# Performance work log

Measured on AMD Instinct MI355X. Metric: run time of the kernel, lower is better.

The kernel has to match this reference:

```python
import jax, jax.numpy as jnp
import numpy as np
import math

IMG_W, IMG_H = 800, 320
N_POINTS = 72
N_STRIPS = 71
S = 36   # sample_points
P = 192  # n_priors
C = 64   # prior_fea_channels == fc_hidden_dim
B = 32

SAMPLE_X_IDX = (np.linspace(0, 1, S) * N_STRIPS).astype(np.int64)
PRIOR_FEAT_YS = np.flip(1.0 - SAMPLE_X_IDX.astype(np.float32) / N_STRIPS).copy()
PRIOR_YS = np.linspace(1, 0, N_POINTS, dtype=np.float32)


def _init_priors():
    emb = np.zeros((P, 3), np.float32)
    left = P // 8
    bottom = P * 3 // 4
    strip = 0.5 / (left // 2 - 1)
    bstrip = 1.0 / (bottom // 4 + 1)
    for i in range(left):
        emb[i] = ((i // 2) * strip, 0.0, 0.16 if i % 2 == 0 else 0.32)
    for i in range(left, left + bottom):
        emb[i] = (0.0, ((i - left) // 4 + 1) * bstrip, 0.2 * (i % 4 + 1))
    for i in range(left + bottom, P):
        emb[i] = (((i - left - bottom) // 2) * strip, 1.0, 0.68 if i % 2 == 0 else 0.84)
    pri = np.zeros((P, 6 + N_POINTS), np.float32)
    pri[:, 2:5] = emb
    pri[:, 6:] = (emb[:, 1:2] * (IMG_W - 1)
                  + (1 - PRIOR_YS[None] - emb[:, 0:1]) * IMG_H / np.tan(emb[:, 2:3] * math.pi + 1e-5)) / (IMG_W - 1)
    return pri.astype(np.float32), pri[:, 6 + SAMPLE_X_IDX].astype(np.float32)


def _bn(x, p):
    # p: (4, C) = gamma, beta, running_mean, running_var; channel axis = 1 (eval mode)
    g, b, m, v = p[0], p[1], p[2], p[3]
    shape = [1] * x.ndim
    shape[1] = -1
    return (x - m.reshape(shape)) * (g.reshape(shape) / jnp.sqrt(v.reshape(shape) + 1e-5)) + b.reshape(shape)


def _conv1d(x, w, pad):
    # x (N, Cin, L), w (Cout, Cin, K); the torch module uses (9,1) conv on (...,36,1)
    return jax.lax.conv_general_dilated(x, w, (1,), [(pad, pad)],
                                        dimension_numbers=('NCH', 'OIH', 'NCH'))


def _grid_sample(img, gx, gy):
    # F.grid_sample: bilinear, align_corners=True, padding_mode='zeros'
    # img (B,C,H,W); gx, gy (B,P,S) in [-1,1] -> out (B,C,P,S)
    b, c, h, w = img.shape
    x = (gx + 1.0) * 0.5 * (w - 1)
    y = (gy + 1.0) * 0.5 * (h - 1)
    x0 = jnp.floor(x)
    y0 = jnp.floor(y)
    imgf = img.reshape(b, c, h * w)

    def gather(xi, yi):
        valid = (xi >= 0) & (xi <= w - 1) & (yi >= 0) & (yi <= h - 1)
        xi_c = jnp.clip(xi, 0, w - 1).astype(jnp.int32)
        yi_c = jnp.clip(yi, 0, h - 1).astype(jnp.int32)
        idx = yi_c * w + xi_c
        v = jax.vmap(lambda f, ix: f[:, ix])(imgf, idx)  # (B,C,P,S)
        return v * valid[:, None].astype(img.dtype)

    wx = x - x0
    wy = y - y0
    return (gather(x0, y0) * ((1 - wx) * (1 - wy))[:, None]
            + gather(x0 + 1, y0) * (wx * (1 - wy))[:, None]
            + gather(x0, y0 + 1) * ((1 - wx) * wy)[:, None]
            + gather(x0 + 1, y0 + 1) * (wx * wy)[:, None])


def _resize_nearest(x, oh, ow):
    # torch F.interpolate default: nearest, idx = floor(i * in / out)
    b, c, h, w = x.shape
    ri = (jnp.arange(oh) * h) // oh
    rj = (jnp.arange(ow) * w) // ow
    return x[:, :, ri][:, :, :, rj]


def _forward(x0, x1, x2, priors0, priors_feat0, conv_w, bn_conv, cat_w0, cat_w1, cat_w2,
             bn_cat, fkey_w, bn_key, fval_w, fval_b, fq_w, fq_b, attnW_w, attnW_b,
             fc_w, fc_b, ln_g, ln_b, mlp_w, mlp_b, reg_w, reg_b, cls_w, cls_b):
    feats = [x2, x1, x0]  # batch_features = x[-3:] reversed -> coarsest first
    b = x0.shape[0]
    prior_ys = jnp.asarray(PRIOR_YS)
    feat_ys = jnp.asarray(PRIOR_FEAT_YS)
    sx_idx = jnp.asarray(SAMPLE_X_IDX)
    priors = jnp.broadcast_to(priors0, (b, P, 6 + N_POINTS))
    priors_feat = jnp.broadcast_to(priors_feat0, (b, P, S))
    cat_ws = [cat_w0, cat_w1, cat_w2]
    stage_rois = []
    preds = []
    for stage in range(3):
        fmap = feats[stage]
        prior_xs = priors_feat[:, :, ::-1]  # torch.flip(dim=2)
        gx = prior_xs * 2.0 - 1.0
        gy = jnp.broadcast_to((feat_ys * 2.0 - 1.0)[None, None, :], (b, P, S))
        pooled = _grid_sample(fmap, gx, gy)                 # (B,C,P,S)
        pooled = pooled.transpose(0, 2, 1, 3).reshape(b * P, C, S)
        stage_rois.append(pooled)
        # ROIGather.roi_fea: per-stage (9,1) conv + BN + ReLU, then cat conv
        trans = [jax.nn.relu(_bn(_conv1d(stage_rois[i], conv_w[i], 4), bn_conv[i]))
                 for i in range(stage + 1)]
        cat = jnp.concatenate(trans, axis=1)
        cat = jax.nn.relu(_bn(_conv1d(cat, cat_ws[stage], 4), bn_cat[stage]))  # (B*P,C,S)
        # fc + LayerNorm + ReLU
        roi = cat.reshape(b * P, C * S) @ fc_w + fc_b
        mu = roi.mean(-1, keepdims=True)
        var = roi.var(-1, keepdims=True)
        roi = (roi - mu) / jnp.sqrt(var + 1e-5) * ln_g + ln_b
        roi = jax.nn.relu(roi).reshape(b, P, C)
        # attention: grouped-conv1d query (per-prior scalar), key/value on resized map
        query = jax.nn.relu(roi * fq_w[None, :, None] + fq_b[None, :, None])
        key = jax.nn.relu(_bn(jnp.einsum('bchw,oc->bohw', fmap, fkey_w), bn_key))
        key = _resize_nearest(key, 10, 25).reshape(b, C, 250)
        value = jnp.einsum('bchw,oc->bohw', fmap, fval_w) + fval_b[None, :, None, None]
        value = _resize_nearest(value, 10, 25).reshape(b, C, 250)
        sim = jax.nn.softmax(jnp.einsum('bpc,bck->bpk', query, key) * (C ** -0.5), axis=-1)
        context = jnp.einsum('bpk,bck->bpc', sim, value)
        context = context * attnW_w[None, :, None] + attnW_b[None, :, None]
        roi = roi + context  # dropout inactive in eval
        # heads (source bug: reg and cls share the SAME Linear applied twice)
        f = roi.reshape(b * P, C)
        h = jax.nn.relu(f @ mlp_w + mlp_b)
        h = jax.nn.relu(h @ mlp_w + mlp_b)
        cls_logits = (h @ cls_w + cls_b).reshape(b, P, 2)
        reg = (h @ reg_w + reg_b).reshape(b, P, 4 + N_POINTS)
        p2 = priors[..., 2] + reg[..., 0]
        p3 = priors[..., 3] + reg[..., 1]
        p4 = priors[..., 4] + reg[..., 2]
        p5 = reg[..., 3]
        geom = (p3[..., None] * (IMG_W - 1)
                + (1.0 - prior_ys[None, None, :] - p2[..., None]) * IMG_H
                / jnp.tan(p4[..., None] * math.pi + 1e-5)) / (IMG_W - 1)
        head = jnp.stack([cls_logits[..., 0], cls_logits[..., 1], p2, p3, p4, p5], axis=-1)
        pred = jnp.concatenate([head, geom + reg[..., 4:]], axis=-1)
        preds.append(pred)
        if stage != 2:
            lines = jax.lax.stop_gradient(jnp.concatenate([head, geom], axis=-1))
            priors = lines
            priors_feat = lines[..., 6 + sx_idx]
    return jnp.stack(preds, axis=0)  # (3, B, P, 78)


def setup_inputs() -> dict:
    key = jax.random.key(0)
    ks = list(jax.random.split(key, 24))
    f32 = jnp.float32
    rn = lambda k, sh, s: jax.random.normal(k, sh, dtype=f32) * s

    def bn_p(k, *lead):
        k1, k2, k3, k4 = jax.random.split(k, 4)
        g = 0.75 + 0.5 * jax.random.uniform(k1, lead + (C,), dtype=f32)
        b = 0.1 * jax.random.normal(k2, lead + (C,), dtype=f32)
        m = 0.1 * jax.random.normal(k3, lead + (C,), dtype=f32)
        v = 0.75 + 0.5 * jax.random.uniform(k4, lead + (C,), dtype=f32)
        return jnp.stack([g, b, m, v], axis=-2)  # (..., 4, C)

    pri, prif = _init_priors()
    return {
        'x0': rn(ks[0], (B, C, IMG_H // 8, IMG_W // 8), 1.0),
        'x1': rn(ks[1], (B, C, IMG_H // 16, IMG_W // 16), 1.0),
        'x2': rn(ks[2], (B, C, IMG_H // 32, IMG_W // 32), 1.0),
        'priors0': jnp.asarray(pri),
        'priors_feat0': jnp.asarray(prif),
        'conv_w': rn(ks[3], (3, C, C, 9), 0.04),
        'bn_conv': bn_p(ks[4], 3),
        'cat_w0': rn(ks[5], (C, C, 9), 0.04),
        'cat_w1': rn(ks[6], (C, 2 * C, 9), 0.03),
        'cat_w2': rn(ks[7], (C, 3 * C, 9), 0.025),
        'bn_cat': bn_p(ks[8], 3),
        'fkey_w': rn(ks[9], (C, C), 0.12),
        'bn_key': bn_p(ks[10]),
        'fval_w': rn(ks[11], (C, C), 0.12),
        'fval_b': rn(ks[12], (C,), 0.05),
        'fq_w': 1.0 + rn(ks[13], (P,), 0.1),
        'fq_b': rn(ks[14], (P,), 0.05),
        'attnW_w': rn(ks[15], (P,), 0.02),
        'attnW_b': rn(ks[16], (P,), 0.02),
        'fc_w': rn(ks[17], (C * S, C), 0.02),
        'fc_b': rn(ks[18], (C,), 0.02),
        'ln_g': jnp.ones((C,), f32),
        'ln_b': jnp.zeros((C,), f32),
        'mlp_w': rn(ks[19], (C, C), 0.12),
        'mlp_b': rn(ks[20], (C,), 0.02),
        'reg_w': rn(ks[21], (C, 4 + N_POINTS), 0.001),
        'reg_b': rn(ks[22], (4 + N_POINTS,), 0.001),
        'cls_w': rn(ks[23], (C, 2), 0.001),
        'cls_b': jnp.zeros((2,), f32),
    }


def reference(x0, x1, x2, priors0, priors_feat0, conv_w, bn_conv, cat_w0, cat_w1, cat_w2,
              bn_cat, fkey_w, bn_key, fval_w, fval_b, fq_w, fq_b, attnW_w, attnW_b,
              fc_w, fc_b, ln_g, ln_b, mlp_w, mlp_b, reg_w, reg_b, cls_w, cls_b):
    return _forward(x0, x1, x2, priors0, priors_feat0, conv_w, bn_conv, cat_w0, cat_w1,
                    cat_w2, bn_cat, fkey_w, bn_key, fval_w, fval_b, fq_w, fq_b,
                    attnW_w, attnW_b, fc_w, fc_b, ln_g, ln_b, mlp_w, mlp_b,
                    reg_w, reg_b, cls_w, cls_b)
```

## Files before the change

kernel.cpp:

```cpp
#include <hip/hip_runtime.h>
#include <hip/hip_bf16.h>
#include <math.h>

typedef __hip_bfloat16 bf16;
typedef __attribute__((ext_vector_type(8))) short short8v;
typedef __attribute__((ext_vector_type(4))) float float4v;

static constexpr int kB = 32;
static constexpr int kP = 192;
static constexpr int kS = 36;
static constexpr int kC = 64;
static constexpr int kRows = kB * kP;
static constexpr float kPI = 3.14159265358979323846f;

__device__ __constant__ int d_SX[36] = {
  0,2,4,6,8,10,12,14,16,18,20,22,24,26,28,30,32,34,
  36,38,40,42,44,46,48,50,52,54,56,58,60,62,64,66,68,71};

__device__ __forceinline__ float b2f(bf16 v) { return __bfloat162float(v); }
__device__ __forceinline__ unsigned short f2bu(float f) {
  bf16 h = __float2bfloat16(f);
  return *reinterpret_cast<unsigned short*>(&h);
}
__device__ __forceinline__ float su2f(unsigned short u) {
  bf16 t; *reinterpret_cast<unsigned short*>(&t) = u; return __bfloat162float(t);
}
#define MFMA16 __builtin_amdgcn_mfma_f32_16x16x32_bf16

__device__ __forceinline__ void wprep_one(
    int d, const float* __restrict__ src, bf16* __restrict__ dst, int CI)
{
  int j   = d & 7;
  int l   = (d >> 3) & 63;
  int wid = (d >> 9) & 3;
  int r   = d >> 11;
  int nchi = CI >> 5;
  int chi = r % nchi, t = r / nchi;
  int co = wid * 16 + (l & 15);
  int ci = chi * 32 + 8 * (l >> 4) + j;
  dst[d] = __float2bfloat16(src[(co * CI + ci) * 9 + t]);
}

__global__ __launch_bounds__(256) void k_prep_all(
    const float* __restrict__ conv_w,
    const float* __restrict__ cat_w0, const float* __restrict__ cat_w1,
    const float* __restrict__ cat_w2,
    const float* __restrict__ fc_w, const float* __restrict__ mlp_w,
    const float* __restrict__ regw, const float* __restrict__ regb,
    const float* __restrict__ clsw, const float* __restrict__ clsb,
    const float* __restrict__ fkeyw, const float* __restrict__ fvalw,
    bf16* __restrict__ wtr0, bf16* __restrict__ wtr1, bf16* __restrict__ wtr2,
    bf16* __restrict__ wcat0, bf16* __restrict__ wcat1, bf16* __restrict__ wcat2,
    bf16* __restrict__ wfc, bf16* __restrict__ mlpwT,
    bf16* __restrict__ rcT, float* __restrict__ rcb,
    float* __restrict__ fkeyT, float* __restrict__ fvalT)
{
  int d = blockIdx.x * 256 + threadIdx.x;
  if (d < 36864)        { wprep_one(d, conv_w,               wtr0, 64); return; }
  d -= 36864;
  if (d < 36864)        { wprep_one(d, conv_w + 36864,       wtr1, 64); return; }
  d -= 36864;
  if (d < 36864)        { wprep_one(d, conv_w + 2*36864,     wtr2, 64); return; }
  d -= 36864;
  if (d < 36864)        { wprep_one(d, cat_w0, wcat0, 64);  return; }
  d -= 36864;
  if (d < 73728)        { wprep_one(d, cat_w1, wcat1, 128); return; }
  d -= 73728;
  if (d < 110592)       { wprep_one(d, cat_w2, wcat2, 192); return; }
  d -= 110592;
  if (d < 147456) {
    int j    = d & 7;
    int l    = (d >> 3) & 63;
    int tile = (d >> 9) & 3;
    int kk   = d >> 11;
    int cout = tile * 16 + (l & 15);
    int k    = kk * 32 + 8 * (l >> 4) + j;
    int c = k & 63, s = k >> 6;
    wfc[d] = __float2bfloat16(fc_w[(c * kS + s) * kC + cout]);
    return;
  }
  d -= 147456;
  if (d < 4096) {
    int co = d >> 6, ci = d & 63;
    mlpwT[d] = __float2bfloat16(mlp_w[ci * 64 + co]);
    return;
  }
  d -= 4096;
  if (d < 5120) {
    int o = d >> 6, ci = d & 63;
    float v = (o < 76) ? regw[ci * 76 + o] : (o < 78 ? clsw[ci * 2 + (o - 76)] : 0.f);
    rcT[d] = __float2bfloat16(v);
    if (d < 80) rcb[d] = (d < 76) ? regb[d] : (d < 78 ? clsb[d - 76] : 0.f);
    return;
  }
  d -= 5120;
  if (d < 4096) {
    int c = d >> 6, co = d & 63;
    fkeyT[d] = fkeyw[co * 64 + c];
    return;
  }
  d -= 4096;
  if (d < 4096) {
    int c = d >> 6, co = d & 63;
    fvalT[d] = fvalw[co * 64 + c];
  }
}

__global__ __launch_bounds__(256) void k_transpose3(
    const float* __restrict__ x2, const float* __restrict__ x1, const float* __restrict__ x0,
    bf16* __restrict__ f0, bf16* __restrict__ f1, bf16* __restrict__ f2)
{
  __shared__ float tile[64][65];
  int byA = blockIdx.x;
  const float* src; bf16* dst; int h, w;
  if (byA < kB*10)            { src = x2; dst = f0; h = 10; w = 25;  }
  else if (byA < kB*30)       { src = x1; dst = f1; h = 20; w = 50;  byA -= kB*10; }
  else                        { src = x0; dst = f2; h = 40; w = 100; byA -= kB*30; }
  const int b = byA / h, y = byA % h;
  const int lane = threadIdx.x & 63, wq = threadIdx.x >> 6;
  for (int x0i = 0; x0i < w; x0i += 64) {
    #pragma unroll
    for (int cc = 0; cc < 16; ++cc) {
      int c = wq * 16 + cc;
      int x = x0i + lane;
      if (x < w) tile[c][lane] = src[((size_t)(b*kC + c)*h + y)*w + x];
    }
    __syncthreads();
    #pragma unroll
    for (int xx = 0; xx < 16; ++xx) {
      int x = x0i + wq * 16 + xx;
      if (x < w) dst[((size_t)(b*h + y)*w + x)*kC + lane] = __float2bfloat16(tile[lane][wq*16 + xx]);
    }
    __syncthreads();
  }
}

__global__ __launch_bounds__(256) void k_keyval3(
    const bf16* __restrict__ f0, const bf16* __restrict__ f1, const bf16* __restrict__ f2,
    const float* __restrict__ fkeyT, const float* __restrict__ bnk,
    const float* __restrict__ fvalT, const float* __restrict__ fvalb,
    bf16* __restrict__ k0, bf16* __restrict__ v0,
    bf16* __restrict__ k1, bf16* __restrict__ v1,
    bf16* __restrict__ k2, bf16* __restrict__ v2)
{
  const int tid = threadIdx.x, lane = tid & 63, grp = tid >> 6;
  int blk = blockIdx.x;
  const int stage = blk / (kB*64);
  blk -= stage * (kB*64);
  const bf16* fmapT; bf16 *key_pc, *val_ck; int h, w;
  if (stage == 0)      { fmapT = f0; key_pc = k0; val_ck = v0; h = 10; w = 25;  }
  else if (stage == 1) { fmapT = f1; key_pc = k1; val_ck = v1; h = 20; w = 50;  }
  else                 { fmapT = f2; key_pc = k2; val_ck = v2; h = 40; w = 100; }
  const int b = blk >> 6, pg = blk & 63;
  const int pos = pg * 4 + grp;
  __shared__ float fv[4][64];
  const bool valid = (pos < 250);
  if (valid) {
    int i = pos / 25, j = pos % 25;
    int yi = (i * h) / 10, xj = (j * w) / 25;
    fv[grp][lane] = b2f(fmapT[((size_t)(b*h + yi)*w + xj)*kC + lane]);
  }
  __syncthreads();
  if (valid) {
    float ka = 0.f, va = 0.f;
    #pragma unroll 8
    for (int c = 0; c < kC; ++c) {
      float f = fv[grp][c];
      ka += f * fkeyT[c*64 + lane];
      va += f * fvalT[c*64 + lane];
    }
    float g = bnk[lane], bb = bnk[kC + lane];
    float m = bnk[2*kC + lane], v = bnk[3*kC + lane];
    float sc = g / sqrtf(v + 1e-5f), sh = bb - m * sc;
    key_pc[((size_t)b*256 + pos)*kC + lane] = __float2bfloat16(fmaxf(ka*sc + sh, 0.f));
    val_ck[((size_t)b*kC + lane)*256 + pos] = __float2bfloat16(va + fvalb[lane]);
  } else {
    key_pc[((size_t)b*256 + pos)*kC + lane] = __float2bfloat16(0.f);
    val_ck[((size_t)b*kC + lane)*256 + pos] = __float2bfloat16(0.f);
  }
}

__global__ __launch_bounds__(256) void k_trans(
    const bf16* __restrict__ fmapT, int h, int w,
    const float* __restrict__ pfeat0, const float* __restrict__ pfeatw, int stage,
    const bf16* __restrict__ wfrag,
    const float* __restrict__ bnp,
    bf16* __restrict__ transOut)
{
  __shared__ __align__(16) bf16 poolT[2][56][64];
  __shared__ float bsc[kC], bsh[kC];
  const int tid = threadIdx.x;
  const int row0 = blockIdx.x * 2, b = row0 / kP;

  if (tid < kC) {
    float g = bnp[tid], bb = bnp[kC + tid];
    float m = bnp[2*kC + tid], v = bnp[3*kC + tid];
    float sc = g / sqrtf(v + 1e-5f);
    bsc[tid] = sc; bsh[tid] = bb - m * sc;
  }
  unsigned int* pz = (unsigned int*)&poolT[0][0][0];
  for (int e = tid; e < 2*56*32; e += 256) pz[e] = 0u;
  __syncthreads();

  const int lc = tid & 7;
  for (int idx = tid >> 3; idx < 2*kS; idx += 32) {
    int r2 = idx / kS, s = idx % kS;
    int row = row0 + r2, p = row % kP;
    float px = (stage == 0) ? pfeat0[p*kS + (kS-1-s)] : pfeatw[row*kS + (kS-1-s)];
    float fy = 1.0f - (float)d_SX[kS-1-s] / 71.0f;
    float x = px * (float)(w - 1);
    float y = fy * (float)(h - 1);
    float x0f = floorf(x), y0f = floorf(y);
    float wx = x - x0f, wy = y - y0f;
    int xi = (int)x0f, yi = (int)y0f;
    float a8[8];
    #pragma unroll
    for (int j = 0; j < 8; ++j) a8[j] = 0.f;
    #pragma unroll
    for (int cy = 0; cy < 2; ++cy) {
      #pragma unroll
      for (int cx = 0; cx < 2; ++cx) {
        int xx = xi + cx, yy = yi + cy;
        if (xx >= 0 && xx < w && yy >= 0 && yy < h) {
          float wgt = (cx ? wx : 1.f - wx) * (cy ? wy : 1.f - wy);
          short8v v = *(const short8v*)&fmapT[((size_t)(b*h + yy)*w + xx)*kC + lc*8];
          #pragma unroll
          for (int j = 0; j < 8; ++j)
            a8[j] += su2f((unsigned short)v[j]) * wgt;
        }
      }
    }
    uint4 pk;
    pk.x = (unsigned)f2bu(a8[0]) | ((unsigned)f2bu(a8[1]) << 16);
    pk.y = (unsigned)f2bu(a8[2]) | ((unsigned)f2bu(a8[3]) << 16);
    pk.z = (unsigned)f2bu(a8[4]) | ((unsigned)f2bu(a8[5]) << 16);
    pk.w = (unsigned)f2bu(a8[6]) | ((unsigned)f2bu(a8[7]) << 16);
    int lr = s + 4;
    *reinterpret_cast<uint4*>(&poolT[r2][lr][((lc + lr) & 7)*8]) = pk;
  }
  __syncthreads();

  const int wv = tid >> 6, lane = tid & 63;
  const int r2 = wv & 1, cp = wv >> 1;
  const int lm = lane & 15, lq = lane >> 4;
  float4v acc[2][3] = {{{0,0,0,0},{0,0,0,0},{0,0,0,0}},{{0,0,0,0},{0,0,0,0},{0,0,0,0}}};
  #pragma unroll
  for (int t = 0; t < 9; ++t) {
    #pragma unroll
    for (int chi = 0; chi < 2; ++chi) {
      short8v a0 = *(const short8v*)&wfrag[(((t*2 + chi)*4 + cp*2 + 0)*64 + lane)*8];
      short8v a1 = *(const short8v*)&wfrag[(((t*2 + chi)*4 + cp*2 + 1)*64 + lane)*8];
      #pragma unroll
      for (int nt = 0; nt < 3; ++nt) {
        int rr = nt*16 + lm + t;
        int sl = chi*4 + lq;
        short8v bb = *(const short8v*)&poolT[r2][rr][((sl + rr) & 7)*8];
        acc[0][nt] = MFMA16(a0, bb, acc[0][nt], 0, 0, 0);
        acc[1][nt] = MFMA16(a1, bb, acc[1][nt], 0, 0, 0);
      }
    }
  }
  #pragma unroll
  for (int c2 = 0; c2 < 2; ++c2) {
    const int c4 = (cp*2 + c2)*16 + 4*lq;
    float s0 = bsc[c4], s1 = bsc[c4+1], s2 = bsc[c4+2], s3 = bsc[c4+3];
    float h0 = bsh[c4], h1 = bsh[c4+1], h2 = bsh[c4+2], h3 = bsh[c4+3];
    #pragma unroll
    for (int nt = 0; nt < 3; ++nt) {
      int s = nt*16 + lm;
      if (s < kS) {
        uint2 pk;
        pk.x = (unsigned)f2bu(fmaxf(acc[c2][nt][0]*s0 + h0, 0.f))
             | ((unsigned)f2bu(fmaxf(acc[c2][nt][1]*s1 + h1, 0.f)) << 16);
        pk.y = (unsigned)f2bu(fmaxf(acc[c2][nt][2]*s2 + h2, 0.f))
             | ((unsigned)f2bu(fmaxf(acc[c2][nt][3]*s3 + h3, 0.f)) << 16);
        *reinterpret_cast<uint2*>(&transOut[((size_t)(row0+r2)*kS + s)*kC + c4]) = pk;
      }
    }
  }
}

template<int NCI>
__global__ __launch_bounds__(256) void k_catconv(
    const bf16* __restrict__ t0, const bf16* __restrict__ t1, const bf16* __restrict__ t2,
    const bf16* __restrict__ wfrag,
    const float* __restrict__ bnp, bf16* __restrict__ catOut)
{
  constexpr int CB = NCI/8;
  __shared__ __align__(16) bf16 poolT[2][56][NCI];
  __shared__ float bsc[kC], bsh[kC];
  const int tid = threadIdx.x;
  const int row0 = blockIdx.x * 2;
  if (tid < kC) {
    float g = bnp[tid], bb = bnp[kC + tid];
    float m = bnp[2*kC + tid], v = bnp[3*kC + tid];
    float sc = g / sqrtf(v + 1e-5f);
    bsc[tid] = sc; bsh[tid] = bb - m * sc;
  }
  unsigned int* pz = (unsigned int*)&poolT[0][0][0];
  for (int e = tid; e < 2*56*NCI/2; e += 256) pz[e] = 0u;
  __syncthreads();

  const bf16* tb[3] = {t0, t1, t2};
  for (int cc = tid; cc < 2*kS*CB; cc += 256) {
    int r2 = cc / (kS*CB), rem = cc % (kS*CB);
    int s = rem / CB, cb = rem % CB;
    int ch = cb * 8, i = ch >> 6, c = ch & 63;
    const short8v* src = (const short8v*)&tb[i][((size_t)(row0+r2)*kS + s)*kC + c];
    int lr = s + 4;
    int sl = (cb & ~7) | ((cb + lr) & 7);
    *(short8v*)&poolT[r2][lr][sl*8] = *src;
  }
  __syncthreads();

  const int wv = tid >> 6, lane = tid & 63;
  const int r2 = wv & 1, cp = wv >> 1;
  const int lm = lane & 15, lq = lane >> 4;
  float4v acc[2][3] = {{{0,0,0,0},{0,0,0,0},{0,0,0,0}},{{0,0,0,0},{0,0,0,0},{0,0,0,0}}};
  #pragma unroll
  for (int t = 0; t < 9; ++t) {
    #pragma unroll
    for (int chi = 0; chi < NCI/32; ++chi) {
      short8v a0 = *(const short8v*)&wfrag[(((t*(NCI/32) + chi)*4 + cp*2 + 0)*64 + lane)*8];
      short8v a1 = *(const short8v*)&wfrag[(((t*(NCI/32) + chi)*4 + cp*2 + 1)*64 + lane)*8];
      #pragma unroll
      for (int nt = 0; nt < 3; ++nt) {
        int rr = nt*16 + lm + t;
        int sl0 = chi*4 + lq;
        int sl = (sl0 & ~7) | ((sl0 + rr) & 7);
        short8v bb = *(const short8v*)&poolT[r2][rr][sl*8];
        acc[0][nt] = MFMA16(a0, bb, acc[0][nt], 0, 0, 0);
        acc[1][nt] = MFMA16(a1, bb, acc[1][nt], 0, 0, 0);
      }
    }
  }
  #pragma unroll
  for (int c2 = 0; c2 < 2; ++c2) {
    const int c4 = (cp*2 + c2)*16 + 4*lq;
    float s0 = bsc[c4], s1 = bsc[c4+1], s2 = bsc[c4+2], s3 = bsc[c4+3];
    float h0 = bsh[c4], h1 = bsh[c4+1], h2 = bsh[c4+2], h3 = bsh[c4+3];
    #pragma unroll
    for (int nt = 0; nt < 3; ++nt) {
      int s = nt*16 + lm;
      if (s < kS) {
        uint2 pk;
        pk.x = (unsigned)f2bu(fmaxf(acc[c2][nt][0]*s0 + h0, 0.f))
             | ((unsigned)f2bu(fmaxf(acc[c2][nt][1]*s1 + h1, 0.f)) << 16);
        pk.y = (unsigned)f2bu(fmaxf(acc[c2][nt][2]*s2 + h2, 0.f))
             | ((unsigned)f2bu(fmaxf(acc[c2][nt][3]*s3 + h3, 0.f)) << 16);
        *reinterpret_cast<uint2*>(&catOut[((size_t)(row0+r2)*kS + s)*kC + c4]) = pk;
      }
    }
  }
}

__global__ __launch_bounds__(256) void k_tail(
    const bf16* __restrict__ catOut, const bf16* __restrict__ wfc,
    const float* __restrict__ fcb, const float* __restrict__ lng, const float* __restrict__ lnb,
    const bf16* __restrict__ key_pc, const bf16* __restrict__ val_ck,
    const float* __restrict__ fqw, const float* __restrict__ fqb,
    const float* __restrict__ aww, const float* __restrict__ awb,
    const bf16* __restrict__ mlpwT, const float* __restrict__ mlpb,
    const bf16* __restrict__ rcT, const float* __restrict__ rcb,
    const float* __restrict__ priors0, const float* __restrict__ priw_in, int stage,
    float* __restrict__ out, float* __restrict__ priw_out, float* __restrict__ pfeat_out)
{
  __shared__ __align__(16) float partS[4][16][68];
  __shared__ __align__(16) float roiL[12][68];
  __shared__ __align__(16) bf16 q[16][72];
  __shared__ __align__(16) bf16 P[16][264];
  __shared__ float rsum[16];
  __shared__ __align__(16) bf16 r2b[16][72];
  __shared__ __align__(16) bf16 h1l[16][72];
  __shared__ __align__(16) bf16 h2l[16][72];
  __shared__ float regc[12][84];
  __shared__ float ev[12][8];

  const int tid = threadIdx.x;
  const int blk = blockIdx.x, b = blk >> 4, tile = blk & 15;
  const int p0 = tile * 12;
  const int lane = tid & 63, wq = tid >> 6;
  const int lm = lane & 15, lq = lane >> 4;
  float (*S)[264] = (float (*)[264])&partS[0][0][0];

  { unsigned* z1 = (unsigned*)&q[0][0];
    for (int e = tid; e < 16*72/2; e += 256) z1[e] = 0u;
    unsigned* z2 = (unsigned*)&r2b[0][0];
    for (int e = tid; e < 16*72/2; e += 256) z2[e] = 0u; }

  {
    float4v fa[4] = {{0,0,0,0},{0,0,0,0},{0,0,0,0},{0,0,0,0}};
    int r0c = p0 + lm; if (r0c > p0 + 11) r0c = p0 + 11;
    const bf16* bb0 = catOut + (size_t)(b*kP + r0c) * 2304 + lq * 8;
    for (int kk = wq * 18; kk < wq * 18 + 18; ++kk) {
      short8v bf0 = *(const short8v*)&bb0[kk * 32];
      #pragma unroll
      for (int t = 0; t < 4; ++t) {
        short8v afrag = *(const short8v*)&wfc[((kk*4 + t)*64 + lane)*8];
        fa[t] = MFMA16(afrag, bf0, fa[t], 0, 0, 0);
      }
    }
    #pragma unroll
    for (int t = 0; t < 4; ++t)
      *(float4v*)&partS[wq][lm][t*16 + lq*4] = fa[t];
  }
  __syncthreads();
  for (int r = wq; r < 12; r += 4) {
    float v = partS[0][r][lane] + partS[1][r][lane] + partS[2][r][lane] + partS[3][r][lane]
            + fcb[lane];
    float s1 = v, s2 = v * v;
    #pragma unroll
    for (int m = 32; m; m >>= 1) { s1 += __shfl_xor(s1, m, 64); s2 += __shfl_xor(s2, m, 64); }
    float mu = s1 * (1.f/64.f);
    float var = s2 * (1.f/64.f) - mu * mu;
    float y = fmaxf((v - mu) * rsqrtf(var + 1e-5f) * lng[lane] + lnb[lane], 0.f);
    roiL[r][lane] = y;
    int p = p0 + r;
    q[r][lane] = __float2bfloat16(fmaxf(y * fqw[p] + fqb[p], 0.f));
  }
  __syncthreads();

  {
    float4v acc[4] = {{0,0,0,0},{0,0,0,0},{0,0,0,0},{0,0,0,0}};
    #pragma unroll
    for (int ks = 0; ks < 2; ++ks) {
      short8v aq0 = *(const short8v*)&q[lm][ks*32 + 8*lq];
      #pragma unroll
      for (int nt = 0; nt < 4; ++nt) {
        int pos = (wq*4 + nt)*16 + lm;
        short8v bk = *(const short8v*)&key_pc[((size_t)(b*256 + pos))*kC + ks*32 + 8*lq];
        acc[nt] = MFMA16(aq0, bk, acc[nt], 0, 0, 0);
      }
    }
    #pragma unroll
    for (int nt = 0; nt < 4; ++nt)
      #pragma unroll
      for (int r = 0; r < 4; ++r)
        S[lq*4 + r][(wq*4 + nt)*16 + lm] = acc[nt][r] * 0.125f;
  }
  __syncthreads();

  {
    int r = tid >> 4, g = tid & 15;
    float mx = -1e30f;
    #pragma unroll 16
    for (int k = 0; k < 16; ++k) { int c = g + 16*k; if (c < 250) mx = fmaxf(mx, S[r][c]); }
    #pragma unroll
    for (int m = 1; m < 16; m <<= 1) mx = fmaxf(mx, __shfl_xor(mx, m, 64));
    float sum = 0.f;
    #pragma unroll 16
    for (int k = 0; k < 16; ++k) {
      int c = g + 16*k;
      float e = 0.f;
      if (c < 250) { e = expf(S[r][c] - mx); sum += e; }
      P[r][c] = __float2bfloat16(e);
    }
    #pragma unroll
    for (int m = 1; m < 16; m <<= 1) sum += __shfl_xor(sum, m, 64);
    if (g == 0) rsum[r] = sum;
  }
  __syncthreads();

  {
    float4v acc = {0,0,0,0};
    #pragma unroll
    for (int ks = 0; ks < 8; ++ks) {
      short8v bv = *(const short8v*)&val_ck[((size_t)(b*kC + wq*16 + lm))*256 + ks*32 + 8*lq];
      short8v ap0 = *(const short8v*)&P[lm][ks*32 + 8*lq];
      acc = MFMA16(ap0, bv, acc, 0, 0, 0);
    }
    #pragma unroll
    for (int r = 0; r < 4; ++r) {
      int pl = lq*4 + r;
      if (pl < 12) {
        int p = p0 + pl, c = wq*16 + lm;
        float ctx = acc[r] / rsum[pl];
        r2b[pl][c] = __float2bfloat16(roiL[pl][c] + ctx * aww[p] + awb[p]);
      }
    }
  }
  __syncthreads();

  {
    float4v acc = {0,0,0,0};
    #pragma unroll
    for (int ks = 0; ks < 2; ++ks) {
      short8v a0 = *(const short8v*)&r2b[lm][ks*32 + 8*lq];
      short8v bw = *(const short8v*)&mlpwT[(wq*16 + lm)*kC + ks*32 + 8*lq];
      acc = MFMA16(a0, bw, acc, 0, 0, 0);
    }
    #pragma unroll
    for (int r = 0; r < 4; ++r) {
      int rw = lq*4 + r, col = wq*16 + lm;
      h1l[rw][col] = __float2bfloat16(fmaxf(acc[r] + mlpb[col], 0.f));
    }
  }
  __syncthreads();
  {
    float4v acc = {0,0,0,0};
    #pragma unroll
    for (int ks = 0; ks < 2; ++ks) {
      short8v a0 = *(const short8v*)&h1l[lm][ks*32 + 8*lq];
      short8v bw = *(const short8v*)&mlpwT[(wq*16 + lm)*kC + ks*32 + 8*lq];
      acc = MFMA16(a0, bw, acc, 0, 0, 0);
    }
    #pragma unroll
    for (int r = 0; r < 4; ++r) {
      int rw = lq*4 + r, col = wq*16 + lm;
      h2l[rw][col] = __float2bfloat16(fmaxf(acc[r] + mlpb[col], 0.f));
    }
  }
  __syncthreads();
  for (int ntile = wq; ntile < 5; ntile += 4) {
    float4v acc = {0,0,0,0};
    #pragma unroll
    for (int ks = 0; ks < 2; ++ks) {
      short8v a0 = *(const short8v*)&h2l[lm][ks*32 + 8*lq];
      short8v bw = *(const short8v*)&rcT[(ntile*16 + lm)*kC + ks*32 + 8*lq];
      acc = MFMA16(a0, bw, acc, 0, 0, 0);
    }
    #pragma unroll
    for (int r = 0; r < 4; ++r) {
      int rw = lq*4 + r, col = ntile*16 + lm;
      if (rw < 12) regc[rw][col] = acc[r] + rcb[col];
    }
  }
  __syncthreads();

  if (tid < 12) {
    int r = tid, p = p0 + r, grow = b*kP + p;
    float pr2, pr3, pr4;
    if (stage == 0) {
      pr2 = priors0[p*78 + 2]; pr3 = priors0[p*78 + 3]; pr4 = priors0[p*78 + 4];
    } else {
      const float* pw = priw_in + (size_t)grow * 78;
      pr2 = pw[2]; pr3 = pw[3]; pr4 = pw[4];
    }
    float p2 = pr2 + regc[r][0], p3 = pr3 + regc[r][1];
    float p4 = pr4 + regc[r][2], p5 = regc[r][3];
    ev[r][0] = p2; ev[r][1] = p3; ev[r][2] = p4; ev[r][3] = p5;
    ev[r][4] = 320.f / tanf(p4 * kPI + 1e-5f);
    ev[r][5] = regc[r][76]; ev[r][6] = regc[r][77];
  }
  __syncthreads();
  for (int e = tid; e < 12*78; e += 256) {
    int r = e / 78, o = e % 78;
    int p = p0 + r, grow = b*kP + p;
    float p2 = ev[r][0], p3 = ev[r][1], t320 = ev[r][4];
    float g = 0.f, v;
    if (o >= 6) g = (p3 * 799.f + ((float)(o-6) / 71.f - p2) * t320) / 799.f;
    if      (o == 0) v = ev[r][5];
    else if (o == 1) v = ev[r][6];
    else if (o == 2) v = p2;
    else if (o == 3) v = p3;
    else if (o == 4) v = ev[r][2];
    else if (o == 5) v = ev[r][3];
    else             v = g + regc[r][4 + (o - 6)];
    out[((size_t)(stage*kB + b)*kP + p) * 78 + o] = v;
    if (stage < 2) priw_out[(size_t)grow*78 + o] = (o < 6) ? v : g;
  }
  if (stage < 2) {
    for (int e = tid; e < 12*kS; e += 256) {
      int r = e / kS, si = e % kS;
      int grow = b*kP + p0 + r;
      float p2 = ev[r][0], p3 = ev[r][1], t320 = ev[r][4];
      pfeat_out[(size_t)grow*kS + si] =
          (p3 * 799.f + ((float)d_SX[si] / 71.f - p2) * t320) / 799.f;
    }
  }
}

extern "C" void kernel_launch(void* const* d_in, const int* in_sizes, int n_in,
                              void* d_out, int out_size, void* d_ws, size_t ws_size,
                              hipStream_t stream) {
  const float* x0      = (const float*)d_in[0];
  const float* x1      = (const float*)d_in[1];
  const float* x2      = (const float*)d_in[2];
  const float* priors0 = (const float*)d_in[3];
  const float* pfeat0  = (const float*)d_in[4];
  const float* conv_w  = (const float*)d_in[5];
  const float* bn_conv = (const float*)d_in[6];
  const float* cat_w[3]= {(const float*)d_in[7], (const float*)d_in[8], (const float*)d_in[9]};
  const float* bn_cat  = (const float*)d_in[10];
  const float* fkey_w  = (const float*)d_in[11];
  const float* bn_key  = (const float*)d_in[12];
  const float* fval_w  = (const float*)d_in[13];
  const float* fval_b  = (const float*)d_in[14];
  const float* fq_w    = (const float*)d_in[15];
  const float* fq_b    = (const float*)d_in[16];
  const float* attnW_w = (const float*)d_in[17];
  const float* attnW_b = (const float*)d_in[18];
  const float* fc_w    = (const float*)d_in[19];
  const float* fc_b    = (const float*)d_in[20];
  const float* ln_g    = (const float*)d_in[21];
  const float* ln_b    = (const float*)d_in[22];
  const float* mlp_w   = (const float*)d_in[23];
  const float* mlp_b   = (const float*)d_in[24];
  const float* reg_w   = (const float*)d_in[25];
  const float* reg_b   = (const float*)d_in[26];
  const float* cls_w   = (const float*)d_in[27];
  const float* cls_b   = (const float*)d_in[28];
  float* out = (float*)d_out;

  char* ws = (char*)d_ws;
  size_t off = 0;
  auto alloc = [&](size_t bytes) { void* pp = ws + off; off += (bytes + 255) & ~(size_t)255; return pp; };
  bf16* trans[3];
  for (int i = 0; i < 3; ++i) trans[i] = (bf16*)alloc((size_t)kRows * 2304 * sizeof(bf16));
  bf16*  catout = (bf16*) alloc((size_t)kRows * 2304 * sizeof(bf16));
  bf16*  key_pc[3]; bf16* val_ck[3];
  for (int i = 0; i < 3; ++i) {
    key_pc[i] = (bf16*)alloc((size_t)kB * 256 * kC * sizeof(bf16));
    val_ck[i] = (bf16*)alloc((size_t)kB * kC * 256 * sizeof(bf16));
  }
  float* priwA  = (float*)alloc((size_t)kRows * 78 * sizeof(float));
  float* priwB  = (float*)alloc((size_t)kRows * 78 * sizeof(float));
  float* pfw    = (float*)alloc((size_t)kRows * kS * sizeof(float));
  bf16* wtr[3], *wcat[3];
  const int catCI[3] = {64, 128, 192};
  for (int i = 0; i < 3; ++i) wtr[i]  = (bf16*)alloc((size_t)64*64*9 * sizeof(bf16));
  for (int i = 0; i < 3; ++i) wcat[i] = (bf16*)alloc((size_t)64*catCI[i]*9 * sizeof(bf16));
  bf16* wfc    = (bf16*)alloc((size_t)2304*64 * sizeof(bf16));
  bf16* mlpwT  = (bf16*)alloc((size_t)64*64 * sizeof(bf16));
  bf16* rcT    = (bf16*)alloc((size_t)80*64 * sizeof(bf16));
  float* rcb   = (float*)alloc((size_t)80 * sizeof(float));
  float* fkeyT = (float*)alloc((size_t)64*64 * sizeof(float));
  float* fvalT = (float*)alloc((size_t)64*64 * sizeof(float));
  const int hd[3] = {10, 20, 40}, wd[3] = {25, 50, 100};
  bf16* fmapT[3];
  for (int i = 0; i < 3; ++i)
    fmapT[i] = (bf16*)alloc((size_t)kB * hd[i] * wd[i] * kC * sizeof(bf16));
  (void)ws_size; (void)in_sizes; (void)n_in; (void)out_size;

  k_prep_all<<<(496640 + 255)/256, 256, 0, stream>>>(
      conv_w, cat_w[0], cat_w[1], cat_w[2], fc_w, mlp_w, reg_w, reg_b, cls_w, cls_b,
      fkey_w, fval_w,
      wtr[0], wtr[1], wtr[2], wcat[0], wcat[1], wcat[2], wfc, mlpwT, rcT, rcb,
      fkeyT, fvalT);
  k_transpose3<<<kB*70, 256, 0, stream>>>(x2, x1, x0, fmapT[0], fmapT[1], fmapT[2]);
  k_keyval3<<<3*kB*64, 256, 0, stream>>>(fmapT[0], fmapT[1], fmapT[2],
                                         fkeyT, bn_key, fvalT, fval_b,
                                         key_pc[0], val_ck[0], key_pc[1], val_ck[1],
                                         key_pc[2], val_ck[2]);

  for (int st = 0; st < 3; ++st) {
    const int h = hd[st], w = wd[st];
    const float* priw_in  = (st == 1) ? priwA : priwB;
    float*       priw_out = (st == 0) ? priwA : priwB;
    k_trans<<<kRows/2, 256, 0, stream>>>(fmapT[st], h, w, pfeat0, pfw, st,
                                         wtr[st], bn_conv + st*4*kC, trans[st]);
    if (st == 0)
      k_catconv<64><<<kRows/2, 256, 0, stream>>>(trans[0], trans[1], trans[2], wcat[0],
                                                 bn_cat + st*4*kC, catout);
    else if (st == 1)
      k_catconv<128><<<kRows/2, 256, 0, stream>>>(trans[0], trans[1], trans[2], wcat[1],
                                                  bn_cat + st*4*kC, catout);
    else
      k_catconv<192><<<kRows/2, 256, 0, stream>>>(trans[0], trans[1], trans[2], wcat[2],
                                                  bn_cat + st*4*kC, catout);
    k_tail<<<kB*16, 256, 0, stream>>>(catout, wfc, fc_b, ln_g, ln_b,
                                      key_pc[st], val_ck[st], fq_w, fq_b, attnW_w, attnW_b,
                                      mlpwT, mlp_b, rcT, rcb,
                                      priors0, priw_in, st, out, priw_out, pfw);
  }
}
```

Baseline: 390.3 us.

## Fuse per-stage sampling conv with concatenation conv in one kernel

Merges the per-stage grid-sample plus 9-tap conv kernel with the following concatenation conv kernel. The freshly computed stage feature stays in shared memory as the last channel block of the concat input. Earlier stages' features are loaded from global memory, and the final stage no longer writes its intermediate feature to global memory. This removes one launch per stage and a global round trip of the transformed features. In exchange the kernel uses more shared memory and registers, which may reduce occupancy.

```diff
diff --git a/kernel.cpp b/kernel.cpp
--- a/kernel.cpp
+++ b/kernel.cpp
@@ -94,16 +94,9 @@
     return;
   }
   d -= 5120;
-  if (d < 4096) {
-    int c = d >> 6, co = d & 63;
-    fkeyT[d] = fkeyw[co * 64 + c];
-    return;
-  }
+  if (d < 4096) { int c = d >> 6, co = d & 63; fkeyT[d] = fkeyw[co * 64 + c]; return; }
   d -= 4096;
-  if (d < 4096) {
-    int c = d >> 6, co = d & 63;
-    fvalT[d] = fvalw[co * 64 + c];
-  }
+  if (d < 4096) { int c = d >> 6, co = d & 63; fvalT[d] = fvalw[co * 64 + c]; }
 }
 
 __global__ __launch_bounds__(256) void k_transpose3(
@@ -180,175 +173,178 @@
   }
 }
 
-__global__ __launch_bounds__(256) void k_trans(
+template<int ST>
+__global__ __launch_bounds__(256) void k_transcat(
     const bf16* __restrict__ fmapT, int h, int w,
-    const float* __restrict__ pfeat0, const float* __restrict__ pfeatw, int stage,
-    const bf16* __restrict__ wfrag,
-    const float* __restrict__ bnp,
-    bf16* __restrict__ transOut)
+    const float* __restrict__ pfeat0, const float* __restrict__ pfeatw,
+    const bf16* __restrict__ wtr,
+    const float* __restrict__ bnpT,
+    const bf16* __restrict__ t0, const bf16* __restrict__ t1,
+    const bf16* __restrict__ wcat,
+    const float* __restrict__ bnpC,
+    bf16* __restrict__ transOut,
+    bf16* __restrict__ catOut)
 {
-  __shared__ __align__(16) bf16 poolT[2][56][64];
-  __shared__ float bsc[kC], bsh[kC];
+  constexpr int NCI = 64 * (ST + 1);
+  __shared__ __align__(16) bf16 pool[2][56][NCI];
+  __shared__ float bscT[64], bshT[64], bscC[64], bshC[64];
   const int tid = threadIdx.x;
   const int row0 = blockIdx.x * 2, b = row0 / kP;
 
-  if (tid < kC) {
-    float g = bnp[tid], bb = bnp[kC + tid];
-    float m = bnp[2*kC + tid], v = bnp[3*kC + tid];
+  if (tid < 64) {
+    float g = bnpT[tid], bb = bnpT[64+tid], m = bnpT[128+tid], v = bnpT[192+tid];
     float sc = g / sqrtf(v + 1e-5f);
-    bsc[tid] = sc; bsh[tid] = bb - m * sc;
-  }
-  unsigned int* pz = (unsigned int*)&poolT[0][0][0];
-  for (int e = tid; e < 2*56*32; e += 256) pz[e] = 0u;
-  __syncthreads();
-
-  const int lc = tid & 7;
-  for (int idx = tid >> 3; idx < 2*kS; idx += 32) {
-    int r2 = idx / kS, s = idx % kS;
-    int row = row0 + r2, p = row % kP;
-    float px = (stage == 0) ? pfeat0[p*kS + (kS-1-s)] : pfeatw[row*kS + (kS-1-s)];
-    float fy = 1.0f - (float)d_SX[kS-1-s] / 71.0f;
-    float x = px * (float)(w - 1);
-    float y = fy * (float)(h - 1);
-    float x0f = floorf(x), y0f = floorf(y);
-    float wx = x - x0f, wy = y - y0f;
-    int xi = (int)x0f, yi = (int)y0f;
-    float a8[8];
-    #pragma unroll
-    for (int j = 0; j < 8; ++j) a8[j] = 0.f;
-    #pragma unroll
-    for (int cy = 0; cy < 2; ++cy) {
+    bscT[tid] = sc; bshT[tid] = bb - m * sc;
+    g = bnpC[tid]; bb = bnpC[64+tid]; m = bnpC[128+tid]; v = bnpC[192+tid];
+    sc = g / sqrtf(v + 1e-5f);
+    bscC[tid] = sc; bshC[tid] = bb - m * sc;
+  }
+  {
+    unsigned* pz = (unsigned*)&pool[0][0][0];
+    constexpr int ND = NCI/2;
+    for (int e = tid; e < 2*20*ND; e += 256) {
+      int r2 = e / (20*ND), rem = e % (20*ND);
+      int pr = rem / ND, cd = rem % ND;
+      int lr = (pr < 4) ? pr : pr + 36;
+      pz[((size_t)r2*56 + lr)*ND + cd] = 0u;
+    }
+  }
+
+  {
+    const int lc = tid & 7;
+    for (int idx = tid >> 3; idx < 2*kS; idx += 32) {
+      int r2 = idx / kS, s = idx % kS;
+      int row = row0 + r2, p = row % kP;
+      float px = (ST == 0) ? pfeat0[p*kS + (kS-1-s)] : pfeatw[row*kS + (kS-1-s)];
+      float fy = 1.0f - (float)d_SX[kS-1-s] / 71.0f;
+      float x = px * (float)(w - 1);
+      float y = fy * (float)(h - 1);
+      float x0f = floorf(x), y0f = floorf(y);
+      float wx = x - x0f, wy = y - y0f;
+      int xi = (int)x0f, yi = (int)y0f;
+      float a8[8];
       #pragma unroll
-      for (int cx = 0; cx < 2; ++cx) {
-        int xx = xi + cx, yy = yi + cy;
-        if (xx >= 0 && xx < w && yy >= 0 && yy < h) {
-          float wgt = (cx ? wx : 1.f - wx) * (cy ? wy : 1.f - wy);
-          short8v v = *(const short8v*)&fmapT[((size_t)(b*h + yy)*w + xx)*kC + lc*8];
-          #pragma unroll
-          for (int j = 0; j < 8; ++j)
-            a8[j] += su2f((unsigned short)v[j]) * wgt;
+      for (int j = 0; j < 8; ++j) a8[j] = 0.f;
+      #pragma unroll
+      for (int cy = 0; cy < 2; ++cy) {
+        #pragma unroll
+        for (int cx = 0; cx < 2; ++cx) {
+          int xx = xi + cx, yy = yi + cy;
+          if (xx >= 0 && xx < w && yy >= 0 && yy < h) {
+            float wgt = (cx ? wx : 1.f - wx) * (cy ? wy : 1.f - wy);
+            short8v v = *(const short8v*)&fmapT[((size_t)(b*h + yy)*w + xx)*kC + lc*8];
+            #pragma unroll
+            for (int j = 0; j < 8; ++j)
+              a8[j] += su2f((unsigned short)v[j]) * wgt;
+          }
         }
       }
-    }
-    uint4 pk;
-    pk.x = (unsigned)f2bu(a8[0]) | ((unsigned)f2bu(a8[1]) << 16);
-    pk.y = (unsigned)f2bu(a8[2]) | ((unsigned)f2bu(a8[3]) << 16);
-    pk.z = (unsigned)f2bu(a8[4]) | ((unsigned)f2bu(a8[5]) << 16);
-    pk.w = (unsigned)f2bu(a8[6]) | ((unsigned)f2bu(a8[7]) << 16);
-    int lr = s + 4;
-    *reinterpret_cast<uint4*>(&poolT[r2][lr][((lc + lr) & 7)*8]) = pk;
+      uint4 pk;
+      pk.x = (unsigned)f2bu(a8[0]) | ((unsigned)f2bu(a8[1]) << 16);
+      pk.y = (unsigned)f2bu(a8[2]) | ((unsigned)f2bu(a8[3]) << 16);
+      pk.z = (unsigned)f2bu(a8[4]) | ((unsigned)f2bu(a8[5]) << 16);
+      pk.w = (unsigned)f2bu(a8[6]) | ((unsigned)f2bu(a8[7]) << 16);
+      int lr = s + 4;
+      int slot = 8*ST + ((lc + lr) & 7);
+      *reinterpret_cast<uint4*>(&pool[r2][lr][slot*8]) = pk;
+    }
+  }
+  if (ST > 0) {
+    const bf16* tb[2] = {t0, t1};
+    constexpr int CBp = 8 * ST;
+    for (int cc = tid; cc < 2*kS*CBp; cc += 256) {
+      int r2 = cc / (kS*CBp), rem = cc % (kS*CBp);
+      int s = rem / CBp, cb = rem % CBp;
+      int ch = cb * 8, i = ch >> 6, c = ch & 63;
+      const short8v* src = (const short8v*)&tb[i][((size_t)(row0+r2)*kS + s)*kC + c];
+      int lr = s + 4;
+      int sl = (cb & ~7) | ((cb + lr) & 7);
+      *(short8v*)&pool[r2][lr][sl*8] = *src;
+    }
   }
   __syncthreads();
 
   const int wv = tid >> 6, lane = tid & 63;
-  const int r2 = wv & 1, cp = wv >> 1;
+  const int r2w = wv & 1, cp = wv >> 1;
   const int lm = lane & 15, lq = lane >> 4;
-  float4v acc[2][3] = {{{0,0,0,0},{0,0,0,0},{0,0,0,0}},{{0,0,0,0},{0,0,0,0},{0,0,0,0}}};
+
+  float4v accT[2][3] = {{{0,0,0,0},{0,0,0,0},{0,0,0,0}},{{0,0,0,0},{0,0,0,0},{0,0,0,0}}};
   #pragma unroll
   for (int t = 0; t < 9; ++t) {
     #pragma unroll
     for (int chi = 0; chi < 2; ++chi) {
-      short8v a0 = *(const short8v*)&wfrag[(((t*2 + chi)*4 + cp*2 + 0)*64 + lane)*8];
-      short8v a1 = *(const short8v*)&wfrag[(((t*2 + chi)*4 + cp*2 + 1)*64 + lane)*8];
+      short8v a0 = *(const short8v*)&wtr[(((t*2 + chi)*4 + cp*2 + 0)*64 + lane)*8];
+      short8v a1 = *(const short8v*)&wtr[(((t*2 + chi)*4 + cp*2 + 1)*64 + lane)*8];
       #pragma unroll
       for (int nt = 0; nt < 3; ++nt) {
         int rr = nt*16 + lm + t;
-        int sl = chi*4 + lq;
-        short8v bb = *(const short8v*)&poolT[r2][rr][((sl + rr) & 7)*8];
-        acc[0][nt] = MFMA16(a0, bb, acc[0][nt], 0, 0, 0);
-        acc[1][nt] = MFMA16(a1, bb, acc[1][nt], 0, 0, 0);
-      }
-    }
-  }
+        int slot = 8*ST + (((chi*4 + lq) + rr) & 7);
+        short8v bb = *(const short8v*)&pool[r2w][rr][slot*8];
+        accT[0][nt] = MFMA16(a0, bb, accT[0][nt], 0, 0, 0);
+        accT[1][nt] = MFMA16(a1, bb, accT[1][nt], 0, 0, 0);
+      }
+    }
+  }
+  __syncthreads();
+
   #pragma unroll
   for (int c2 = 0; c2 < 2; ++c2) {
     const int c4 = (cp*2 + c2)*16 + 4*lq;
-    float s0 = bsc[c4], s1 = bsc[c4+1], s2 = bsc[c4+2], s3 = bsc[c4+3];
-    float h0 = bsh[c4], h1 = bsh[c4+1], h2 = bsh[c4+2], h3 = bsh[c4+3];
+    float s0 = bscT[c4], s1 = bscT[c4+1], s2 = bscT[c4+2], s3 = bscT[c4+3];
+    float h0 = bshT[c4], h1 = bshT[c4+1], h2 = bshT[c4+2], h3 = bshT[c4+3];
     #pragma unroll
     for (int nt = 0; nt < 3; ++nt) {
       int s = nt*16 + lm;
       if (s < kS) {
         uint2 pk;
-        pk.x = (unsigned)f2bu(fmaxf(acc[c2][nt][0]*s0 + h0, 0.f))
-             | ((unsigned)f2bu(fmaxf(acc[c2][nt][1]*s1 + h1, 0.f)) << 16);
-        pk.y = (unsigned)f2bu(fmaxf(acc[c2][nt][2]*s2 + h2, 0.f))
-             | ((unsigned)f2bu(fmaxf(acc[c2][nt][3]*s3 + h3, 0.f)) << 16);
-        *reinterpret_cast<uint2*>(&transOut[((size_t)(row0+r2)*kS + s)*kC + c4]) = pk;
-      }
-    }
-  }
-}
-
-template<int NCI>
-__global__ __launch_bounds__(256) void k_catconv(
-    const bf16* __restrict__ t0, const bf16* __restrict__ t1, const bf16* __restrict__ t2,
-    const bf16* __restrict__ wfrag,
-    const float* __restrict__ bnp, bf16* __restrict__ catOut)
-{
-  constexpr int CB = NCI/8;
-  __shared__ __align__(16) bf16 poolT[2][56][NCI];
-  __shared__ float bsc[kC], bsh[kC];
-  const int tid = threadIdx.x;
-  const int row0 = blockIdx.x * 2;
-  if (tid < kC) {
-    float g = bnp[tid], bb = bnp[kC + tid];
-    float m = bnp[2*kC + tid], v = bnp[3*kC + tid];
-    float sc = g / sqrtf(v + 1e-5f);
-    bsc[tid] = sc; bsh[tid] = bb - m * sc;
-  }
-  unsigned int* pz = (unsigned int*)&poolT[0][0][0];
-  for (int e = tid; e < 2*56*NCI/2; e += 256) pz[e] = 0u;
-  __syncthreads();
-
-  const bf16* tb[3] = {t0, t1, t2};
-  for (int cc = tid; cc < 2*kS*CB; cc += 256) {
-    int r2 = cc / (kS*CB), rem = cc % (kS*CB);
-    int s = rem / CB, cb = rem % CB;
-    int ch = cb * 8, i = ch >> 6, c = ch & 63;
-    const short8v* src = (const short8v*)&tb[i][((size_t)(row0+r2)*kS + s)*kC + c];
-    int lr = s + 4;
-    int sl = (cb & ~7) | ((cb + lr) & 7);
-    *(short8v*)&poolT[r2][lr][sl*8] = *src;
-  }
-  __syncthreads();
-
-  const int wv = tid >> 6, lane = tid & 63;
-  const int r2 = wv & 1, cp = wv >> 1;
-  const int lm = lane & 15, lq = lane >> 4;
-  float4v acc[2][3] = {{{0,0,0,0},{0,0,0,0},{0,0,0,0}},{{0,0,0,0},{0,0,0,0},{0,0,0,0}}};
+        pk.x = (unsigned)f2bu(fmaxf(accT[c2][nt][0]*s0 + h0, 0.f))
+             | ((unsigned)f2bu(fmaxf(accT[c2][nt][1]*s1 + h1, 0.f)) << 16);
+        pk.y = (unsigned)f2bu(fmaxf(accT[c2][nt][2]*s2 + h2, 0.f))
+             | ((unsigned)f2bu(fmaxf(accT[c2][nt][3]*s3 + h3, 0.f)) << 16);
+        if (ST < 2)
+          *reinterpret_cast<uint2*>(&transOut[((size_t)(row0+r2w)*kS + s)*kC + c4]) = pk;
+        int ch = 64*ST + c4;
+        int cb2 = ch >> 3, lr = s + 4;
+        int sl = (cb2 & ~7) | ((cb2 + lr) & 7);
+        *reinterpret_cast<uint2*>(&pool[r2w][lr][sl*8 + (ch & 7)]) = pk;
+      }
+    }
+  }
+  __syncthreads();
+
+  float4v accC[2][3] = {{{0,0,0,0},{0,0,0,0},{0,0,0,0}},{{0,0,0,0},{0,0,0,0},{0,0,0,0}}};
   #pragma unroll
   for (int t = 0; t < 9; ++t) {
     #pragma unroll
     for (int chi = 0; chi < NCI/32; ++chi) {
-      short8v a0 = *(const short8v*)&wfrag[(((t*(NCI/32) + chi)*4 + cp*2 + 0)*64 + lane)*8];
-      short8v a1 = *(const short8v*)&wfrag[(((t*(NCI/32) + chi)*4 + cp*2 + 1)*64 + lane)*8];
+      short8v a0 = *(const short8v*)&wcat[(((t*(NCI/32) + chi)*4 + cp*2 + 0)*64 + lane)*8];
+      short8v a1 = *(const short8v*)&wcat[(((t*(NCI/32) + chi)*4 + cp*2 + 1)*64 + lane)*8];
       #pragma unroll
       for (int nt = 0; nt < 3; ++nt) {
         int rr = nt*16 + lm + t;
         int sl0 = chi*4 + lq;
         int sl = (sl0 & ~7) | ((sl0 + rr) & 7);
-        short8v bb = *(const short8v*)&poolT[r2][rr][sl*8];
-        acc[0][nt] = MFMA16(a0, bb, acc[0][nt], 0, 0, 0);
-        acc[1][nt] = MFMA16(a1, bb, acc[1][nt], 0, 0, 0);
+        short8v bb = *(const short8v*)&pool[r2w][rr][sl*8];
+        accC[0][nt] = MFMA16(a0, bb, accC[0][nt], 0, 0, 0);
+        accC[1][nt] = MFMA16(a1, bb, accC[1][nt], 0, 0, 0);
       }
     }
   }
   #pragma unroll
   for (int c2 = 0; c2 < 2; ++c2) {
     const int c4 = (cp*2 + c2)*16 + 4*lq;
-    float s0 = bsc[c4], s1 = bsc[c4+1], s2 = bsc[c4+2], s3 = bsc[c4+3];
-    float h0 = bsh[c4], h1 = bsh[c4+1], h2 = bsh[c4+2], h3 = bsh[c4+3];
+    float s0 = bscC[c4], s1 = bscC[c4+1], s2 = bscC[c4+2], s3 = bscC[c4+3];
+    float h0 = bshC[c4], h1 = bshC[c4+1], h2 = bshC[c4+2], h3 = bshC[c4+3];
     #pragma unroll
     for (int nt = 0; nt < 3; ++nt) {
       int s = nt*16 + lm;
       if (s < kS) {
         uint2 pk;
-        pk.x = (unsigned)f2bu(fmaxf(acc[c2][nt][0]*s0 + h0, 0.f))
-             | ((unsigned)f2bu(fmaxf(acc[c2][nt][1]*s1 + h1, 0.f)) << 16);
-        pk.y = (unsigned)f2bu(fmaxf(acc[c2][nt][2]*s2 + h2, 0.f))
-             | ((unsigned)f2bu(fmaxf(acc[c2][nt][3]*s3 + h3, 0.f)) << 16);
-        *reinterpret_cast<uint2*>(&catOut[((size_t)(row0+r2)*kS + s)*kC + c4]) = pk;
+        pk.x = (unsigned)f2bu(fmaxf(accC[c2][nt][0]*s0 + h0, 0.f))
+             | ((unsigned)f2bu(fmaxf(accC[c2][nt][1]*s1 + h1, 0.f)) << 16);
+        pk.y = (unsigned)f2bu(fmaxf(accC[c2][nt][2]*s2 + h2, 0.f))
+             | ((unsigned)f2bu(fmaxf(accC[c2][nt][3]*s3 + h3, 0.f)) << 16);
+        *reinterpret_cast<uint2*>(&catOut[((size_t)(row0+r2w)*kS + s)*kC + c4]) = pk;
       }
     }
   }
@@ -605,8 +601,8 @@
   char* ws = (char*)d_ws;
   size_t off = 0;
   auto alloc = [&](size_t bytes) { void* pp = ws + off; off += (bytes + 255) & ~(size_t)255; return pp; };
-  bf16* trans[3];
-  for (int i = 0; i < 3; ++i) trans[i] = (bf16*)alloc((size_t)kRows * 2304 * sizeof(bf16));
+  bf16* trans[2];
+  for (int i = 0; i < 2; ++i) trans[i] = (bf16*)alloc((size_t)kRows * 2304 * sizeof(bf16));
   bf16*  catout = (bf16*) alloc((size_t)kRows * 2304 * sizeof(bf16));
   bf16*  key_pc[3]; bf16* val_ck[3];
   for (int i = 0; i < 3; ++i) {
@@ -643,24 +639,28 @@
                                          key_pc[0], val_ck[0], key_pc[1], val_ck[1],
                                          key_pc[2], val_ck[2]);
 
-  for (int st = 0; st < 3; ++st) {
-    const int h = hd[st], w = wd[st];
-    const float* priw_in  = (st == 1) ? priwA : priwB;
-    float*       priw_out = (st == 0) ? priwA : priwB;
-    k_trans<<<kRows/2, 256, 0, stream>>>(fmapT[st], h, w, pfeat0, pfw, st,
-                                         wtr[st], bn_conv + st*4*kC, trans[st]);
-    if (st == 0)
-      k_catconv<64><<<kRows/2, 256, 0, stream>>>(trans[0], trans[1], trans[2], wcat[0],
-                                                 bn_cat + st*4*kC, catout);
-    else if (st == 1)
-      k_catconv<128><<<kRows/2, 256, 0, stream>>>(trans[0], trans[1], trans[2], wcat[1],
-                                                  bn_cat + st*4*kC, catout);
-    else
-      k_catconv<192><<<kRows/2, 256, 0, stream>>>(trans[0], trans[1], trans[2], wcat[2],
-                                                  bn_cat + st*4*kC, catout);
-    k_tail<<<kB*16, 256, 0, stream>>>(catout, wfc, fc_b, ln_g, ln_b,
-                                      key_pc[st], val_ck[st], fq_w, fq_b, attnW_w, attnW_b,
-                                      mlpwT, mlp_b, rcT, rcb,
-                                      priors0, priw_in, st, out, priw_out, pfw);
-  }
-}
+  k_transcat<0><<<kRows/2, 256, 0, stream>>>(fmapT[0], hd[0], wd[0], pfeat0, pfw,
+                                             wtr[0], bn_conv + 0*256,
+                                             trans[0], trans[1], wcat[0], bn_cat + 0*256,
+                                             trans[0], catout);
+  k_tail<<<kB*16, 256, 0, stream>>>(catout, wfc, fc_b, ln_g, ln_b,
+                                    key_pc[0], val_ck[0], fq_w, fq_b, attnW_w, attnW_b,
+                                    mlpwT, mlp_b, rcT, rcb,
+                                    priors0, priwB, 0, out, priwA, pfw);
+  k_transcat<1><<<kRows/2, 256, 0, stream>>>(fmapT[1], hd[1], wd[1], pfeat0, pfw,
+                                             wtr[1], bn_conv + 1*256,
+                                             trans[0], trans[1], wcat[1], bn_cat + 1*256,
+                                             trans[1], catout);
+  k_tail<<<kB*16, 256, 0, stream>>>(catout, wfc, fc_b, ln_g, ln_b,
+                                    key_pc[1], val_ck[1], fq_w, fq_b, attnW_w, attnW_b,
+                                    mlpwT, mlp_b, rcT, rcb,
+                                    priors0, priwA, 1, out, priwB, pfw);
+  k_transcat<2><<<kRows/2, 256, 0, stream>>>(fmapT[2], hd[2], wd[2], pfeat0, pfw,
+                                             wtr[2], bn_conv + 2*256,
+                                             trans[0], trans[1], wcat[2], bn_cat + 2*256,
+                                             nullptr, catout);
+  k_tail<<<kB*16, 256, 0, stream>>>(catout, wfc, fc_b, ln_g, ln_b,
+                                    key_pc[2], val_ck[2], fq_w, fq_b, attnW_w, attnW_b,
+                                    mlpwT, mlp_b, rcT, rcb,
+                                    priors0, priwB, 2, out, priwA, pfw);
+}
```

Measured after the change: 399.8 us. +2.4%, slower.
